# Performance work log

Hardware: AMD Instinct MI355X
Metric: run time of the kernel (lower is better)

Reference implementation:

```python
import jax, jax.numpy as jnp
import numpy as np

B, T, N, H = 16, 49, 24, 256
S = 0.05  # init scale (keeps sigmoids/tanh out of saturation for numeric testing)


def setup_inputs() -> dict:
    key = jax.random.key(0)
    ks = jax.random.split(key, 16)
    rn = lambda k, shp: (jax.random.normal(k, shp, dtype=jnp.float32) * S)
    return dict(
        h=rn(ks[0], (B, T, N, H)),
        c_h=rn(ks[1], (B, T, N, H)),
        p=rn(ks[2], (B, T, N, H)),
        g_t=rn(ks[3], (B, T, N, H)),
        c_g_t=rn(ks[4], (B, T, N, H)),
        g_s=rn(ks[5], (B, T, N, H)),
        c_g_s=rn(ks[6], (B, T, N, H)),
        # 9 h-gates stacked in order: i, lt, ft, rt, s, gt, gs, o, c
        U=rn(ks[7], (9, N, H, H)),
        Wt=rn(ks[8], (9, N, 3 * H, H)),
        Ws=rn(ks[9], (9, N, H, H)),
        Zt=rn(ks[10], (9, N, H, H)),
        Zs=rn(ks[11], (9, N, H, H)),
        b=rn(ks[12], (9, N, 1, H)),
        # 6 global gates stacked in order: gtf, gtg, gto, gsf, gsg, gso
        Wg=rn(ks[13], (6, N, H, H)),
        Zg=rn(ks[14], (6, N, H, H)),
        bg=rn(ks[15], (6, N, 1, H)),
        train=1,
    )


def _cell(h, c_h, p, g_t, c_g_t, g_s, c_g_s, U, Wt, Ws, Zt, Zs, b, Wg, Zg, bg):
    pad_t = jnp.zeros_like(h[:, :, :1, :])
    pad_s = jnp.zeros_like(h[:, :1, :, :])
    # spatial (bone) neighbours along axis 2
    h_t_before = jnp.concatenate([pad_t, h[:, :, :-1, :]], axis=2)
    h_t_after = jnp.concatenate([h[:, :, 1:, :], pad_t], axis=2)
    h_tba = jnp.concatenate([h_t_before, h, h_t_after], axis=3)  # [B,T,N,3H]
    c_t_before = jnp.concatenate([pad_t, c_h[:, :, :-1, :]], axis=2)
    c_t_after = jnp.concatenate([c_h[:, :, 1:, :], pad_t], axis=2)
    # temporal predecessor along axis 1
    h_s_before = jnp.concatenate([pad_s, h[:, :-1, :, :]], axis=1)
    c_s_before = jnp.concatenate([pad_s, c_h[:, :-1, :, :]], axis=1)

    # Faithful quirk of the source: f_ft gate uses Zslt (the lt gate's Zs) for its g_s term.
    Zs_eff = Zs.at[2].set(Zs[1])

    # All 9 gate preactivations in one fused batched-GEMM pass: [9,B,T,N,H]
    pre = (jnp.einsum('btnh,gnhk->gbtnk', p, U)
           + jnp.einsum('btnm,gnmk->gbtnk', h_tba, Wt)
           + jnp.einsum('btnh,gnhk->gbtnk', h_s_before, Ws)
           + jnp.einsum('btnh,gnhk->gbtnk', g_t, Zt)
           + jnp.einsum('btnh,gnhk->gbtnk', g_s, Zs_eff)
           + b[:, None, None, :, 0, :])
    i_n, f_lt, f_ft, f_rt, f_s, f_gt, f_gs, o_n = jax.nn.sigmoid(pre[:8])
    c_n = jnp.tanh(pre[8])

    c_h_new = (f_lt * c_t_before + f_ft * c_h + f_rt * c_t_after
               + f_s * c_s_before + f_gt * c_g_t + f_gs * c_g_s + i_n * c_n)
    h_new = o_n * jnp.tanh(c_h_new)

    def _global(x_g, c_g, Wg3, Zg3, bg3):
        pre_g = (jnp.einsum('btnh,gnhk->gbtnk', h_new, Wg3)
                 + jnp.einsum('btnh,gnhk->gbtnk', x_g, Zg3)
                 + bg3[:, None, None, :, 0, :])
        f_g = jax.nn.sigmoid(pre_g[0])
        cand = jnp.tanh(pre_g[1])
        o_g = jax.nn.sigmoid(pre_g[2])
        c_g_new = f_g * c_g + (1.0 - f_g) * cand
        return o_g * jnp.tanh(c_g_new), c_g_new

    g_t_new, c_g_t_new = _global(g_t, c_g_t, Wg[:3], Zg[:3], bg[:3])
    g_s_new, c_g_s_new = _global(g_s, c_g_s, Wg[3:], Zg[3:], bg[3:])
    return h_new, c_h_new, g_t_new, c_g_t_new, g_s_new, c_g_s_new


def reference(h, c_h, p, g_t, c_g_t, g_s, c_g_s, U, Wt, Ws, Zt, Zs, b, Wg, Zg, bg, train):
    # `train` is a flag unused by the cell's math (kept for signature fidelity)
    return _cell(h, c_h, p, g_t, c_g_t, g_s, c_g_s, U, Wt, Ws, Zt, Zs, b, Wg, Zg, bg)
```

## Files before the change

kernel.cpp:

```cpp
#include <hip/hip_runtime.h>
#include <hip/hip_bf16.h>

typedef unsigned short u16;
typedef u16 u16x8 __attribute__((ext_vector_type(8)));
typedef short s16x8 __attribute__((ext_vector_type(8)));
typedef float f32x4 __attribute__((ext_vector_type(4)));
typedef unsigned int u32;

#define NN 24
#define TT 49
#define MR 784
#define SZT 4816896

__device__ inline u16 f2b(float f){
    __hip_bfloat16 b = __float2bfloat16(f); u16 r; __builtin_memcpy(&r, &b, 2); return r;
}
__device__ inline float sig_(float x){ return 1.f / (1.f + __expf(-x)); }
__device__ inline float tanh_(float x){ float e = __expf(2.f * x); return (e - 1.f) / (e + 1.f); }

__device__ inline void gld16(const u16* g, u16* l){
    __builtin_amdgcn_global_load_lds(
        (const __attribute__((address_space(1))) unsigned int*)g,
        (__attribute__((address_space(3))) unsigned int*)l, 16, 0, 0);
}

#define BAR()      __builtin_amdgcn_s_barrier()
#define WAITVM(N)  asm volatile("s_waitcnt vmcnt(" #N ")" ::: "memory")
#define WAITVL(N)  asm volatile("s_waitcnt vmcnt(" #N ") lgkmcnt(0)" ::: "memory")

#define WT0_ELEMS ((size_t)216 * 256 * 1792)
#define WT1_ELEMS ((size_t)144 * 256 * 512)

__global__ __launch_bounds__(256) void prep_all(
    const float* __restrict__ U,  const float* __restrict__ Wt,
    const float* __restrict__ Ws, const float* __restrict__ Zt,
    const float* __restrict__ Zs, const float* __restrict__ Wg,
    const float* __restrict__ Zg,
    const float* __restrict__ p,  const float* __restrict__ h,
    const float* __restrict__ g_t, const float* __restrict__ g_s,
    u16* __restrict__ wt0, u16* __restrict__ wt1, u16* __restrict__ Abf)
{
    __shared__ u16 T[64][72];
    const int tid = threadIdx.x;
    const int lin = blockIdx.x;

    if (lin < 24192) {
        const int kt = lin % 28, ct = (lin / 28) % 4, z = lin / 112;
        const int n = z % NN, g = z / NN;
        const int k0 = kt * 64;
        const float* wbase;
        if (k0 < 256)       wbase = U  + (size_t)((g * NN + n) * 256 + k0)          * 256;
        else if (k0 < 1024) wbase = Wt + (size_t)((g * NN + n) * 768 + (k0 - 256))  * 256;
        else if (k0 < 1280) wbase = Ws + (size_t)((g * NN + n) * 256 + (k0 - 1024)) * 256;
        else if (k0 < 1536) wbase = Zt + (size_t)((g * NN + n) * 256 + (k0 - 1280)) * 256;
        else { const int g2 = (g == 2) ? 1 : g;
               wbase = Zs + (size_t)((g2 * NN + n) * 256 + (k0 - 1536)) * 256; }
        const int colg = ct * 64 + (tid & 15) * 4;
        #pragma unroll
        for (int it = 0; it < 4; ++it) {
            const int krl = (tid >> 4) + it * 16;
            const float4 v = *(const float4*)(wbase + (size_t)krl * 256 + colg);
            const int cl = (tid & 15) * 4;
            T[cl + 0][krl] = f2b(v.x); T[cl + 1][krl] = f2b(v.y);
            T[cl + 2][krl] = f2b(v.z); T[cl + 3][krl] = f2b(v.w);
        }
        __syncthreads();
        const int col_l = tid >> 2, ks = (tid & 3) * 16;
        const int ktile = 2 * kt + (ks >> 5);
        const int koff  = ks & 31;
        u16* dst = wt0 + (size_t)z * 458752 + (size_t)ktile * 8192
                       + (size_t)(ct * 64 + col_l) * 32 + koff;
        u16x8 w0, w1;
        #pragma unroll
        for (int j2 = 0; j2 < 8; ++j2) { w0[j2] = T[col_l][ks + j2]; w1[j2] = T[col_l][ks + 8 + j2]; }
        *(u16x8*)(dst) = w0; *(u16x8*)(dst + 8) = w1;
    } else if (lin < 28800) {
        const int l = lin - 24192;
        const int kt = l % 8, ct = (l / 8) % 4, z = l / 32;
        const int k0 = kt * 64;
        const float* wbase = (k0 < 256)
            ? Wg + (size_t)(z * 256 + k0) * 256
            : Zg + (size_t)(z * 256 + (k0 - 256)) * 256;
        const int colg = ct * 64 + (tid & 15) * 4;
        #pragma unroll
        for (int it = 0; it < 4; ++it) {
            const int krl = (tid >> 4) + it * 16;
            const float4 v = *(const float4*)(wbase + (size_t)krl * 256 + colg);
            const int cl = (tid & 15) * 4;
            T[cl + 0][krl] = f2b(v.x); T[cl + 1][krl] = f2b(v.y);
            T[cl + 2][krl] = f2b(v.z); T[cl + 3][krl] = f2b(v.w);
        }
        __syncthreads();
        const int col_l = tid >> 2, ks = (tid & 3) * 16;
        const int ktile = 2 * kt + (ks >> 5);
        const int koff  = ks & 31;
        u16* dst = wt1 + (size_t)z * 131072 + (size_t)ktile * 8192
                       + (size_t)(ct * 64 + col_l) * 32 + koff;
        u16x8 w0, w1;
        #pragma unroll
        for (int j2 = 0; j2 < 8; ++j2) { w0[j2] = T[col_l][ks + j2]; w1[j2] = T[col_l][ks + 8 + j2]; }
        *(u16x8*)(dst) = w0; *(u16x8*)(dst + 8) = w1;
    } else {
        const int l = lin - 28800;
        const int bx = l % 13, kt = (l / 13) % 56, n = l / 728;
        const int row = bx * 64 + (tid >> 2);
        if (row >= MR) return;
        const int c  = tid & 3;
        const int kg = kt * 32 + c * 8;
        const int seg = kg >> 8, koff = kg & 255;
        const int ec = (row * NN + n) * 256 + koff;
        const float* src = nullptr; bool valid = true;
        switch (seg) {
            case 0: src = p + ec; break;
            case 1: valid = (n > 0);          src = h + ec - 256; break;
            case 2: src = h + ec; break;
            case 3: valid = (n < NN - 1);     src = h + ec + 256; break;
            case 4: valid = (row % TT) != 0;  src = h + ec - NN * 256; break;
            case 5: src = g_t + ec; break;
            default: src = g_s + ec; break;
        }
        float4 lo = {0.f,0.f,0.f,0.f}, hi = lo;
        if (valid) { lo = *(const float4*)src; hi = *(const float4*)(src + 4); }
        u16x8 w;
        w[0] = f2b(lo.x); w[1] = f2b(lo.y); w[2] = f2b(lo.z); w[3] = f2b(lo.w);
        w[4] = f2b(hi.x); w[5] = f2b(hi.y); w[6] = f2b(hi.z); w[7] = f2b(hi.w);
        *(u16x8*)(Abf + ((size_t)(n * 56 + kt) * MR + row) * 32 + c * 8) = w;
    }
}

#define ABUF9 3584
#define BBUF9 18432
#define BUFE9 (ABUF9 + BBUF9)

__global__ __launch_bounds__(512, 1) void fused_cell9(
    const float* __restrict__ c_h, const float* __restrict__ c_g_t,
    const float* __restrict__ c_g_s,
    const u16* __restrict__ Abf, const u16* __restrict__ WT0,
    const float* __restrict__ Bias,
    float* __restrict__ h_new, float* __restrict__ c_h_new)
{
    extern __shared__ u16 smem[];

    const int tid = threadIdx.x;
    const int lin = blockIdx.x;
    const int xcd = lin & 7, jj = lin >> 3;
    const int mtile = jj % 7;
    const int slab  = (jj / 7) * 8 + xcd;
    const int ntile = slab & 3, n = slab >> 2;

    const int wave = tid >> 6, lane = tid & 63;
    const int rh = wave >> 2, cq = wave & 3;
    const int lrow = lane & 15, lci = lane >> 4;
    const int MC = (rh == 0) ? 4 : 3;

    const int rloc = (wave < 7) ? (wave * 16 + (lane >> 2)) : 0;
    const int ach  = (lane & 3) ^ ((rloc >> 1) & 3);
    const u16* aSrc = Abf + ((size_t)(n * 56) * MR + mtile * 112 + rloc) * 32 + ach * 8;
    const int aDst = wave * 512 + lane * 8;

    const int ng = (wave < 4) ? 5 : 4;
    const u16* bSrc[5]; int bDst[5];
    #pragma unroll
    for (int i = 0; i < 5; ++i) {
        const int G = (i < ng) ? (wave + 8 * i) : 0;
        const int g = G >> 2, q = G & 3;
        const int c = q * 16 + (lane >> 2);
        const int ch = (lane & 3) ^ ((c >> 1) & 3);
        bSrc[i] = WT0 + (size_t)n * 458752 + (size_t)g * 11010048
                + (size_t)(ntile * 64 + c) * 32 + ch * 8;
        bDst[i] = ABUF9 + g * 2048 + q * 512 + lane * 8;
    }

    int aro[4];
    #pragma unroll
    for (int m = 0; m < 4; ++m) {
        const int row = rh * 64 + m * 16 + lrow;
        aro[m] = row * 32 + ((lci ^ ((row >> 1) & 3)) << 3);
    }
    const int colr = cq * 16 + lrow;
    const int bro  = ABUF9 + colr * 32 + ((lci ^ ((colr >> 1) & 3)) << 3);

    f32x4 acc[9][4];
    #pragma unroll
    for (int g = 0; g < 9; ++g)
        #pragma unroll
        for (int m = 0; m < 4; ++m) acc[g][m] = f32x4{0.f, 0.f, 0.f, 0.f};

    auto dma = [&](int kt, int buf) {
        u16* base = smem + buf * BUFE9;
        if (wave < 7) gld16(aSrc + (size_t)kt * (MR * 32), base + aDst);
        const size_t ko = (size_t)kt * 8192;
        #pragma unroll
        for (int i = 0; i < 5; ++i)
            if (i < ng) gld16(bSrc[i] + ko, base + bDst[i]);
    };
    auto waitw = [&]() {
        if (wave < 4)      { WAITVM(6); }
        else if (wave < 7) { WAITVM(5); }
        else               { WAITVM(4); }
    };
    auto domfma = [&](int buf) {
        const u16* base = smem + buf * BUFE9;
        s16x8 af[4];
        #pragma unroll
        for (int m = 0; m < 4; ++m)
            if (m < MC) af[m] = *(const s16x8*)(&base[aro[m]]);
        __builtin_amdgcn_s_setprio(1);
        #pragma unroll
        for (int g = 0; g < 9; ++g) {
            const s16x8 bf = *(const s16x8*)(&base[g * 2048 + bro]);
            #pragma unroll
            for (int m = 0; m < 4; ++m)
                if (m < MC)
                    acc[g][m] = __builtin_amdgcn_mfma_f32_16x16x32_bf16(af[m], bf, acc[g][m], 0, 0, 0);
        }
        __builtin_amdgcn_s_setprio(0);
    };

    dma(0, 0); dma(1, 1);
    waitw(); BAR();
    for (int t3 = 0; t3 < 54; t3 += 3) {
        dma(t3 + 2, 2); domfma(0); waitw(); BAR();
        dma(t3 + 3, 0); domfma(1); waitw(); BAR();
        dma(t3 + 4, 1); domfma(2); waitw(); BAR();
    }
    domfma(0);
    WAITVM(0); BAR();
    domfma(1);

    const int col = ntile * 64 + cq * 16 + lrow;
    float bv[9];
    #pragma unroll
    for (int g = 0; g < 9; ++g) bv[g] = Bias[(g * NN + n) * 256 + col];

    #pragma unroll
    for (int m = 0; m < 4; ++m) {
        if (m < MC) {
            #pragma unroll
            for (int i = 0; i < 4; ++i) {
                const int row = mtile * 112 + rh * 64 + m * 16 + (lane >> 4) * 4 + i;
                const size_t e = ((size_t)(row * NN + n)) * 256 + col;
                const float i_n  = sig_(acc[0][m][i] + bv[0]);
                const float f_lt = sig_(acc[1][m][i] + bv[1]);
                const float f_ft = sig_(acc[2][m][i] + bv[2]);
                const float f_rt = sig_(acc[3][m][i] + bv[3]);
                const float f_s  = sig_(acc[4][m][i] + bv[4]);
                const float f_gt = sig_(acc[5][m][i] + bv[5]);
                const float f_gs = sig_(acc[6][m][i] + bv[6]);
                const float o_n  = sig_(acc[7][m][i] + bv[7]);
                const float c_n  = tanh_(acc[8][m][i] + bv[8]);
                const float cb = (n > 0)      ? c_h[e - 256] : 0.f;
                const float ca = (n < NN - 1) ? c_h[e + 256] : 0.f;
                const float cs = (row % TT)   ? c_h[e - NN * 256] : 0.f;
                const float cn = f_lt * cb + f_ft * c_h[e] + f_rt * ca
                               + f_s * cs + f_gt * c_g_t[e] + f_gs * c_g_s[e]
                               + i_n * c_n;
                c_h_new[e] = cn;
                h_new[e]   = o_n * tanh_(cn);
            }
        }
    }
}

__global__ __launch_bounds__(256, 4) void fused_global5(
    const float* __restrict__ hn,   const float* __restrict__ g_t,
    const float* __restrict__ g_s,  const float* __restrict__ c_g_t,
    const float* __restrict__ c_g_s,
    const u16* __restrict__ WT1, const float* __restrict__ Bg,
    float* __restrict__ out2, float* __restrict__ out3,
    float* __restrict__ out4, float* __restrict__ out5)
{
    __shared__ u16 smem[2 * 2048 + 2 * 6144];

    const int tid = threadIdx.x;
    const int lin = blockIdx.x;
    const int xcd = lin & 7, j = lin >> 3;
    const int mtile = j % 13;
    const int slab  = (j / 13) * 8 + xcd;
    const int ntile = slab & 3;
    const int zz    = slab >> 2;
    const int n = zz % NN, grp = zz / NN;

    const float* xg = grp ? g_s : g_t;
    const float* cg = grp ? c_g_s : c_g_t;
    float* og  = grp ? out4 : out2;
    float* ocg = grp ? out5 : out3;

    const int s_r = tid >> 2, s_c = tid & 3;
    const int gr  = mtile * 64 + s_r;
    const bool mval = (gr < MR);
    const int ec = (gr * NN + n) * 256;

    const int wro = s_r * 32 + ((s_c ^ ((s_r >> 1) & 3)) << 3);

    const int wave = tid >> 6, lane = tid & 63;
    const int lrow = lane & 15, lci = lane >> 4;

    int aro[4];
    #pragma unroll
    for (int m = 0; m < 4; ++m) {
        const int row = m * 16 + lrow;
        aro[m] = row * 32 + ((lci ^ ((row >> 1) & 3)) << 3);
    }
    const int colr = wave * 16 + lrow;
    const int bro  = colr * 32 + ((lci ^ ((colr >> 1) & 3)) << 3);

    const u16* wbase = WT1 + (size_t)(grp * 3 * NN + n) * 131072
                           + (size_t)(ntile * 64) * 32 + wro;

    f32x4 acc[3][4];
    #pragma unroll
    for (int g = 0; g < 3; ++g)
        #pragma unroll
        for (int m = 0; m < 4; ++m) acc[g][m] = f32x4{0.f, 0.f, 0.f, 0.f};

    float4 aOlo, aOhi, aNlo, aNhi;

    auto loadA = [&](int kt, float4& lo, float4& hi) {
        const int K0 = kt * 32, koff = (K0 & 255) + s_c * 8;
        const float* src = ((K0 < 256) ? hn : xg) + ec + koff;
        lo = make_float4(0.f, 0.f, 0.f, 0.f); hi = lo;
        if (mval) { lo = *(const float4*)src; hi = *(const float4*)(src + 4); }
    };
    auto storeA = [&](int buf, const float4& lo, const float4& hi) {
        u16x8 aw;
        aw[0] = f2b(lo.x); aw[1] = f2b(lo.y); aw[2] = f2b(lo.z); aw[3] = f2b(lo.w);
        aw[4] = f2b(hi.x); aw[5] = f2b(hi.y); aw[6] = f2b(hi.z); aw[7] = f2b(hi.w);
        *(u16x8*)(&smem[buf * 2048 + wro]) = aw;
    };
    auto dmaB = [&](int kt, int buf) {
        const u16* wb = wbase + (size_t)kt * 8192;
        u16* dst = &smem[2 * 2048 + buf * 6144 + tid * 8];
        #pragma unroll
        for (int g = 0; g < 3; ++g)
            gld16(wb + (size_t)g * 3145728, dst + g * 2048);
    };
    auto domfma = [&](int buf) {
        const u16* Asb = smem + buf * 2048;
        const u16* Bsb = smem + 2 * 2048 + buf * 6144;
        s16x8 af[4];
        #pragma unroll
        for (int m = 0; m < 4; ++m) af[m] = *(const s16x8*)(&Asb[aro[m]]);
        __builtin_amdgcn_s_setprio(1);
        #pragma unroll
        for (int g = 0; g < 3; ++g) {
            const s16x8 bf = *(const s16x8*)(&Bsb[g * 2048 + bro]);
            #pragma unroll
            for (int m = 0; m < 4; ++m)
                acc[g][m] = __builtin_amdgcn_mfma_f32_16x16x32_bf16(af[m], bf, acc[g][m], 0, 0, 0);
        }
        __builtin_amdgcn_s_setprio(0);
    };

    loadA(0, aOlo, aOhi);
    dmaB(0, 0);
    storeA(0, aOlo, aOhi);
    loadA(1, aOlo, aOhi);
    dmaB(1, 1);
    WAITVL(5); BAR();
    for (int kt = 0; kt < 14; kt += 2) {
        domfma(0);
        BAR();
        loadA(kt + 2, aNlo, aNhi);
        dmaB(kt + 2, 0);
        storeA(1, aOlo, aOhi);
        WAITVL(5); BAR();
        domfma(1);
        BAR();
        loadA(kt + 3, aOlo, aOhi);
        dmaB(kt + 3, 1);
        storeA(0, aNlo, aNhi);
        WAITVL(5); BAR();
    }
    domfma(0);
    BAR();
    storeA(1, aOlo, aOhi);
    WAITVL(0); BAR();
    domfma(1);

    const int col = ntile * 64 + wave * 16 + lrow;
    float bv[3];
    #pragma unroll
    for (int g = 0; g < 3; ++g) bv[g] = Bg[((grp * 3 + g) * NN + n) * 256 + col];

    #pragma unroll
    for (int m = 0; m < 4; ++m) {
        #pragma unroll
        for (int i = 0; i < 4; ++i) {
            const int row = mtile * 64 + m * 16 + (lane >> 4) * 4 + i;
            if (row < MR) {
                const size_t e = ((size_t)(row * NN + n)) * 256 + col;
                const float f    = sig_(acc[0][m][i] + bv[0]);
                const float cand = tanh_(acc[1][m][i] + bv[1]);
                const float o    = sig_(acc[2][m][i] + bv[2]);
                const float cn = f * cg[e] + (1.f - f) * cand;
                ocg[e] = cn;
                og[e]  = o * tanh_(cn);
            }
        }
    }
}

extern "C" void kernel_launch(void* const* d_in, const int* in_sizes, int n_in,
                              void* d_out, int out_size, void* d_ws, size_t ws_size,
                              hipStream_t stream)
{
    const float* h     = (const float*)d_in[0];
    const float* c_h   = (const float*)d_in[1];
    const float* p     = (const float*)d_in[2];
    const float* g_t   = (const float*)d_in[3];
    const float* c_g_t = (const float*)d_in[4];
    const float* g_s   = (const float*)d_in[5];
    const float* c_g_s = (const float*)d_in[6];
    const float* U     = (const float*)d_in[7];
    const float* Wt    = (const float*)d_in[8];
    const float* Ws    = (const float*)d_in[9];
    const float* Zt    = (const float*)d_in[10];
    const float* Zs    = (const float*)d_in[11];
    const float* bb    = (const float*)d_in[12];
    const float* Wg    = (const float*)d_in[13];
    const float* Zg    = (const float*)d_in[14];
    const float* bg    = (const float*)d_in[15];

    float* out0 = (float*)d_out;
    float* out1 = out0 + (size_t)SZT;
    float* out2 = out1 + (size_t)SZT;
    float* out3 = out2 + (size_t)SZT;
    float* out4 = out3 + (size_t)SZT;
    float* out5 = out4 + (size_t)SZT;

    u16* wt0 = (u16*)d_ws;
    u16* wt1 = wt0 + WT0_ELEMS;
    u16* abf = wt1 + WT1_ELEMS;

    dim3 blk(256);
    prep_all<<<dim3(46272), blk, 0, stream>>>(U, Wt, Ws, Zt, Zs, Wg, Zg,
                                              p, h, g_t, g_s, wt0, wt1, abf);

    const int ldsBytes = 3 * BUFE9 * (int)sizeof(u16);
    hipFuncSetAttribute((const void*)fused_cell9,
                        hipFuncAttributeMaxDynamicSharedMemorySize, ldsBytes);
    fused_cell9<<<dim3(672), dim3(512), ldsBytes, stream>>>(
        c_h, c_g_t, c_g_s, abf, wt0, bb, out0, out1);
    fused_global5<<<dim3(2496), blk, 0, stream>>>(
        out0, g_t, g_s, c_g_t, c_g_s, wt1, bg, out2, out3, out4, out5);
}
```

Measured before the change: 452.5 us.

## Halve N-tile of fused cell GEMM to 32 columns with 256-thread blocks

The main gate GEMM kernel moves from 64-column tiles in 512-thread blocks to 32-column tiles in 256-thread blocks, with two blocks per CU and twice as many blocks. The A and B DMA assignments, the LDS buffer sizes and the wait counts are redistributed across 4 waves. The aim is more blocks in flight so that one block's epilogue and memory stalls overlap with another block's MFMA work. In exchange, each A tile is now loaded from global memory twice as often, which lowers data reuse per block.

Result: no change. 448.6 us (-0.9%).

```diff
diff --git a/kernel.cpp b/kernel.cpp
--- a/kernel.cpp
+++ b/kernel.cpp
@@ -128,11 +128,11 @@
     }
 }
 
-#define ABUF9 3584
-#define BBUF9 18432
-#define BUFE9 (ABUF9 + BBUF9)
-
-__global__ __launch_bounds__(512, 1) void fused_cell9(
+#define AB10 3584
+#define BB10 9216
+#define BUFE10 (AB10 + BB10)
+
+__global__ __launch_bounds__(256, 2) void fused_cell10(
     const float* __restrict__ c_h, const float* __restrict__ c_g_t,
     const float* __restrict__ c_g_s,
     const u16* __restrict__ Abf, const u16* __restrict__ WT0,
@@ -146,30 +146,32 @@
     const int xcd = lin & 7, jj = lin >> 3;
     const int mtile = jj % 7;
     const int slab  = (jj / 7) * 8 + xcd;
-    const int ntile = slab & 3, n = slab >> 2;
+    const int ntile = slab & 7, n = slab >> 3;
 
     const int wave = tid >> 6, lane = tid & 63;
-    const int rh = wave >> 2, cq = wave & 3;
+    const int rh = wave >> 1, cq = wave & 1;
     const int lrow = lane & 15, lci = lane >> 4;
     const int MC = (rh == 0) ? 4 : 3;
 
-    const int rloc = (wave < 7) ? (wave * 16 + (lane >> 2)) : 0;
-    const int ach  = (lane & 3) ^ ((rloc >> 1) & 3);
-    const u16* aSrc = Abf + ((size_t)(n * 56) * MR + mtile * 112 + rloc) * 32 + ach * 8;
-    const int aDst = wave * 512 + lane * 8;
-
-    const int ng = (wave < 4) ? 5 : 4;
-    const u16* bSrc[5]; int bDst[5];
-    #pragma unroll
-    for (int i = 0; i < 5; ++i) {
-        const int G = (i < ng) ? (wave + 8 * i) : 0;
-        const int g = G >> 2, q = G & 3;
-        const int c = q * 16 + (lane >> 2);
-        const int ch = (lane & 3) ^ ((c >> 1) & 3);
-        bSrc[i] = WT0 + (size_t)n * 458752 + (size_t)g * 11010048
-                + (size_t)(ntile * 64 + c) * 32 + ch * 8;
-        bDst[i] = ABUF9 + g * 2048 + q * 512 + lane * 8;
-    }
+    const int nga = (wave < 3) ? 2 : 1;
+    const u16* aSrc[2]; int aDst[2];
+    #pragma unroll
+    for (int i = 0; i < 2; ++i) {
+        const int a = (i < nga) ? (wave + 4 * i) : 0;
+        const int r = a * 16 + (lane >> 2);
+        const int ach = (lane & 3) ^ ((r >> 1) & 3);
+        aSrc[i] = Abf + ((size_t)(n * 56) * MR + mtile * 112 + r) * 32 + ach * 8;
+        aDst[i] = a * 512 + lane * 8;
+    }
+
+    const int ngb = (wave < 2) ? 5 : 4;
+    const int qb  = wave & 1;
+    const int cb  = qb * 16 + (lane >> 2);
+    const int chb = (lane & 3) ^ ((cb >> 1) & 3);
+    const u16* bBase = WT0 + (size_t)n * 458752
+                     + (size_t)(ntile * 32 + cb) * 32 + chb * 8;
+    const int bDst0 = AB10 + qb * 512 + lane * 8;
+    const int gb0 = wave >> 1;
 
     int aro[4];
     #pragma unroll
@@ -178,7 +180,7 @@
         aro[m] = row * 32 + ((lci ^ ((row >> 1) & 3)) << 3);
     }
     const int colr = cq * 16 + lrow;
-    const int bro  = ABUF9 + colr * 32 + ((lci ^ ((colr >> 1) & 3)) << 3);
+    const int bro  = AB10 + colr * 32 + ((lci ^ ((colr >> 1) & 3)) << 3);
 
     f32x4 acc[9][4];
     #pragma unroll
@@ -187,20 +189,24 @@
         for (int m = 0; m < 4; ++m) acc[g][m] = f32x4{0.f, 0.f, 0.f, 0.f};
 
     auto dma = [&](int kt, int buf) {
-        u16* base = smem + buf * BUFE9;
-        if (wave < 7) gld16(aSrc + (size_t)kt * (MR * 32), base + aDst);
-        const size_t ko = (size_t)kt * 8192;
+        u16* base = smem + buf * BUFE10;
+        const size_t koA = (size_t)kt * (MR * 32);
+        #pragma unroll
+        for (int i = 0; i < 2; ++i)
+            if (i < nga) gld16(aSrc[i] + koA, base + aDst[i]);
+        const size_t koB = (size_t)kt * 8192;
         #pragma unroll
         for (int i = 0; i < 5; ++i)
-            if (i < ng) gld16(bSrc[i] + ko, base + bDst[i]);
+            if (i < ngb) gld16(bBase + koB + (size_t)(gb0 + 2 * i) * 11010048,
+                               base + bDst0 + (gb0 + 2 * i) * 1024);
     };
     auto waitw = [&]() {
-        if (wave < 4)      { WAITVM(6); }
-        else if (wave < 7) { WAITVM(5); }
-        else               { WAITVM(4); }
+        if (wave < 2)       { WAITVM(7); }
+        else if (wave == 2) { WAITVM(6); }
+        else                { WAITVM(5); }
     };
     auto domfma = [&](int buf) {
-        const u16* base = smem + buf * BUFE9;
+        const u16* base = smem + buf * BUFE10;
         s16x8 af[4];
         #pragma unroll
         for (int m = 0; m < 4; ++m)
@@ -208,7 +214,7 @@
         __builtin_amdgcn_s_setprio(1);
         #pragma unroll
         for (int g = 0; g < 9; ++g) {
-            const s16x8 bf = *(const s16x8*)(&base[g * 2048 + bro]);
+            const s16x8 bf = *(const s16x8*)(&base[g * 1024 + bro]);
             #pragma unroll
             for (int m = 0; m < 4; ++m)
                 if (m < MC)
@@ -228,7 +234,7 @@
     WAITVM(0); BAR();
     domfma(1);
 
-    const int col = ntile * 64 + cq * 16 + lrow;
+    const int col = ntile * 32 + cq * 16 + lrow;
     float bv[9];
     #pragma unroll
     for (int g = 0; g < 9; ++g) bv[g] = Bias[(g * NN + n) * 256 + col];
@@ -249,11 +255,11 @@
                 const float f_gs = sig_(acc[6][m][i] + bv[6]);
                 const float o_n  = sig_(acc[7][m][i] + bv[7]);
                 const float c_n  = tanh_(acc[8][m][i] + bv[8]);
-                const float cb = (n > 0)      ? c_h[e - 256] : 0.f;
-                const float ca = (n < NN - 1) ? c_h[e + 256] : 0.f;
-                const float cs = (row % TT)   ? c_h[e - NN * 256] : 0.f;
-                const float cn = f_lt * cb + f_ft * c_h[e] + f_rt * ca
-                               + f_s * cs + f_gt * c_g_t[e] + f_gs * c_g_s[e]
+                const float cb_ = (n > 0)      ? c_h[e - 256] : 0.f;
+                const float ca_ = (n < NN - 1) ? c_h[e + 256] : 0.f;
+                const float cs_ = (row % TT)   ? c_h[e - NN * 256] : 0.f;
+                const float cn = f_lt * cb_ + f_ft * c_h[e] + f_rt * ca_
+                               + f_s * cs_ + f_gt * c_g_t[e] + f_gs * c_g_s[e]
                                + i_n * c_n;
                 c_h_new[e] = cn;
                 h_new[e]   = o_n * tanh_(cn);
@@ -437,10 +443,10 @@
     prep_all<<<dim3(46272), blk, 0, stream>>>(U, Wt, Ws, Zt, Zs, Wg, Zg,
                                               p, h, g_t, g_s, wt0, wt1, abf);
 
-    const int ldsBytes = 3 * BUFE9 * (int)sizeof(u16);
-    hipFuncSetAttribute((const void*)fused_cell9,
+    const int ldsBytes = 3 * BUFE10 * (int)sizeof(u16);
+    hipFuncSetAttribute((const void*)fused_cell10,
                         hipFuncAttributeMaxDynamicSharedMemorySize, ldsBytes);
-    fused_cell9<<<dim3(672), dim3(512), ldsBytes, stream>>>(
+    fused_cell10<<<dim3(1344), blk, ldsBytes, stream>>>(
         c_h, c_g_t, c_g_s, abf, wt0, bb, out0, out1);
     fused_global5<<<dim3(2496), blk, 0, stream>>>(
         out0, g_t, g_s, c_g_t, c_g_s, wt1, bg, out2, out3, out4, out5);
```
